# Optimization experiments

Hardware: AMD Instinct MI355X
Metric: run time of the kernel (lower is better)

Reference implementation:

```python
import jax, jax.numpy as jnp
import numpy as np
from math import log

MODEL_DIM = 512
NUM_HEADS = 8
DIM_HEAD = 64
INNER = NUM_HEADS * DIM_HEAD
B, L = 8, 1024
EPS = 1e-5


def setup_inputs() -> dict:
    key = jax.random.key(0)
    ks = jax.random.split(key, 9)
    x = jax.random.normal(ks[0], (B, L, MODEL_DIM), dtype=jnp.float32)
    gamma = jnp.ones((MODEL_DIM,), jnp.float32)
    beta = jnp.zeros((MODEL_DIM,), jnp.float32)
    w_qkv = jax.random.normal(ks[1], (3 * INNER, MODEL_DIM), jnp.float32) * (MODEL_DIM ** -0.5)
    b_qkv = jnp.zeros((3 * INNER,), jnp.float32)
    w_pos = jax.random.normal(ks[2], (INNER, MODEL_DIM), jnp.float32) * (MODEL_DIM ** -0.5)
    w_out = jax.random.normal(ks[3], (MODEL_DIM, INNER), jnp.float32) * (INNER ** -0.5)
    b_out = jnp.zeros((MODEL_DIM,), jnp.float32)
    # xavier_uniform for (num_heads, dim_head)
    bound = (6.0 / (NUM_HEADS + DIM_HEAD)) ** 0.5
    u_bias = jax.random.uniform(ks[4], (NUM_HEADS, DIM_HEAD), jnp.float32, -bound, bound)
    v_bias = jax.random.uniform(ks[5], (NUM_HEADS, DIM_HEAD), jnp.float32, -bound, bound)
    return {"x": x, "gamma": gamma, "beta": beta, "w_qkv": w_qkv, "b_qkv": b_qkv,
            "w_pos": w_pos, "w_out": w_out, "b_out": b_out, "u_bias": u_bias, "v_bias": v_bias}


def _rel_pos_emb(seq_len, d):
    # (L, D): (i - j) scaled by sinusoid frequencies, then cos on even cols, sin on odd cols
    rel = (jnp.arange(seq_len, dtype=jnp.float32)[:, None]
           - jnp.arange(d, dtype=jnp.float32)[None, :])
    freqs = jnp.exp(-jnp.arange(0, 2 * d, 2, dtype=jnp.float32) * (log(10000.0) / MODEL_DIM))
    angle = rel * freqs[None, :]
    even = (jnp.arange(d) % 2) == 0
    return jnp.where(even[None, :], jnp.cos(angle), jnp.sin(angle))  # (L, D)


def reference(x, gamma, beta, w_qkv, b_qkv, w_pos, w_out, b_out, u_bias, v_bias):
    b, l, d = x.shape
    h, dh = NUM_HEADS, DIM_HEAD
    # LayerNorm
    mu = jnp.mean(x, axis=-1, keepdims=True)
    var = jnp.mean(jnp.square(x - mu), axis=-1, keepdims=True)
    xn = (x - mu) * jax.lax.rsqrt(var + EPS) * gamma + beta
    # relative position embedding, identical per batch element
    pe = _rel_pos_emb(l, d)                      # (L, D)
    pos = (pe @ w_pos.T).reshape(l, h, dh)       # (L, H, Dh)
    pos = jnp.transpose(pos, (1, 0, 2))          # (H, L, Dh)
    # qkv
    qkv = xn @ w_qkv.T + b_qkv                   # (B, L, 3*inner)
    q, k, v = jnp.split(qkv, 3, axis=-1)
    def to_heads(t):
        return jnp.transpose(t.reshape(b, l, h, dh), (0, 2, 1, 3))  # (B,H,L,Dh)
    q, k, v = to_heads(q), to_heads(k), to_heads(v)
    scale = dh ** -0.5
    content = jnp.einsum('bhld,bhmd->bhlm', q + u_bias[None, :, None, :], k)
    pos_score = jnp.einsum('bhld,hmd->bhlm', q + v_bias[None, :, None, :], pos)
    attn = jax.nn.softmax((content + pos_score) * scale, axis=-1)
    out = jnp.einsum('bhlm,bhmd->bhld', attn, v)
    out = jnp.transpose(out, (0, 2, 1, 3)).reshape(b, l, h * dh)
    return out @ w_out.T + b_out  # dropout p=0.0 -> identity
```

## Files before the change

kernel.cpp:

```cpp
#include <hip/hip_runtime.h>
#include <math.h>

static constexpr int Bn = 8, Ln = 1024, Dm = 512, Hn = 8, DhN = 64;

typedef short bf16x8 __attribute__((ext_vector_type(8)));
typedef float f32x4 __attribute__((ext_vector_type(4)));
typedef _Float16 f16x4 __attribute__((ext_vector_type(4)));
typedef _Float16 f16x8 __attribute__((ext_vector_type(8)));
typedef unsigned int u32x4 __attribute__((ext_vector_type(4)));

#define QSCALE 0.1803368801111137f

static __device__ __forceinline__ unsigned short f2b(float f) {
  union { float f; unsigned int u; } x;
  x.f = f;
  unsigned int u = x.u;
  unsigned int r = (u + 0x7FFFu + ((u >> 16) & 1u)) >> 16;
  return (unsigned short)r;
}
static __device__ __forceinline__ float b2f(unsigned short u) {
  union { unsigned int u; float f; } x;
  x.u = ((unsigned int)u) << 16;
  return x.f;
}

#define GLDS16(g, l)                                                        \
  __builtin_amdgcn_global_load_lds((const __attribute__((address_space(1))) void*)(g), \
                                   (__attribute__((address_space(3))) void*)(l), 16, 0, 0)

__global__ __launch_bounds__(256) void prep1(const float* __restrict__ x,
                                             const float* __restrict__ gamma,
                                             const float* __restrict__ beta,
                                             unsigned short* __restrict__ xn,
                                             unsigned short* __restrict__ pe,
                                             const float* __restrict__ wq, unsigned short* __restrict__ wqb,
                                             const float* __restrict__ wp, unsigned short* __restrict__ wpb,
                                             const float* __restrict__ wo, unsigned short* __restrict__ wob) {
  int b = blockIdx.x;
  int t = threadIdx.x;
  if (b < 8192) {
    const float2 v = *(const float2*)(x + (size_t)b * Dm + t * 2);
    float s = v.x + v.y;
    float sq = v.x * v.x + v.y * v.y;
#pragma unroll
    for (int off = 32; off > 0; off >>= 1) {
      s += __shfl_down(s, off);
      sq += __shfl_down(sq, off);
    }
    __shared__ float red[8];
    int wave = t >> 6, lane = t & 63;
    if (lane == 0) { red[wave * 2] = s; red[wave * 2 + 1] = sq; }
    __syncthreads();
    float S = red[0] + red[2] + red[4] + red[6];
    float SQ = red[1] + red[3] + red[5] + red[7];
    float mu = S * (1.0f / Dm);
    float var = SQ * (1.0f / Dm) - mu * mu;
    float rstd = rsqrtf(var + 1e-5f);
    int c = t * 2;
    ushort2 o;
    o.x = f2b((v.x - mu) * rstd * gamma[c] + beta[c]);
    o.y = f2b((v.y - mu) * rstd * gamma[c + 1] + beta[c + 1]);
    *(ushort2*)(xn + (size_t)b * Dm + c) = o;
  } else if (b < 10240) {
    int idx = (b - 8192) * 256 + t;
    int l = idx >> 9, k = idx & 511;
    float freq = expf(-0.0359778921f * (float)k);
    float angle = (float)(l - k) * freq;
    pe[idx] = f2b((k & 1) ? sinf(angle) : cosf(angle));
  } else {
    int cb = b - 10240;
    const float* src;
    unsigned short* dst;
    int off;
    if (cb < 768) { src = wq; dst = wqb; off = cb; }
    else if (cb < 1024) { src = wp; dst = wpb; off = cb - 768; }
    else { src = wo; dst = wob; off = cb - 1024; }
    int i = off * 256 + t;
    float4 v = *(const float4*)(src + (size_t)i * 4);
    ushort4 o;
    o.x = f2b(v.x); o.y = f2b(v.y); o.z = f2b(v.z); o.w = f2b(v.w);
    *(ushort4*)(dst + (size_t)i * 4) = o;
  }
}

__global__ __launch_bounds__(256, 8) void gemm_mfma(const unsigned short* __restrict__ Ain,
                                                    const unsigned short* __restrict__ Bwin,
                                                    const float* __restrict__ biasin,
                                                    float* __restrict__ outfin,
                                                    unsigned short* __restrict__ oq,
                                                    unsigned short* __restrict__ ok,
                                                    unsigned short* __restrict__ ov,
                                                    const unsigned short* __restrict__ A2,
                                                    const unsigned short* __restrict__ B2,
                                                    float* __restrict__ outf2,
                                                    int K, int mode) {
  int by = blockIdx.y, bx = blockIdx.x;
  const unsigned short* A = Ain;
  const unsigned short* Bw = Bwin;
  const float* bias = biasin;
  float* outf = outfin;
  if (by >= 128) {
    if (bx >= 8) return;
    A = A2; Bw = B2; bias = nullptr; outf = outf2; mode = 1; by -= 128;
  }
  __shared__ alignas(16) unsigned short As[64 * 64];
  __shared__ alignas(16) unsigned short Bs[64 * 64];
  const int t = threadIdx.x;
  const int lane = t & 63, w = t >> 6;
  const int c = lane & 15, q8 = lane >> 4;
  const int wm = (w & 1) * 32, wn = (w >> 1) * 32;
  const int m0 = by * 64, n0 = bx * 64;

  f32x4 acc[2][2];
#pragma unroll
  for (int i = 0; i < 2; ++i)
#pragma unroll
    for (int j = 0; j < 2; ++j) acc[i][j] = (f32x4){0.f, 0.f, 0.f, 0.f};

  const int srow = lane >> 3;
  const int sgr = (lane & 7) ^ srow;

  for (int k0 = 0; k0 < K; k0 += 64) {
    __syncthreads();
#pragma unroll
    for (int j = 0; j < 2; ++j) {
      int r = j * 32 + w * 8 + srow;
      GLDS16(A + (size_t)(m0 + r) * K + k0 + sgr * 8, As + (j * 256 + w * 64 + lane) * 8);
      GLDS16(Bw + (size_t)(n0 + r) * K + k0 + sgr * 8, Bs + (j * 256 + w * 64 + lane) * 8);
    }
    __syncthreads();
#pragma unroll
    for (int kk = 0; kk < 2; ++kk) {
      bf16x8 a[2], b[2];
      const int q = kk * 4 + q8;
#pragma unroll
      for (int i = 0; i < 2; ++i) {
        int r = wm + i * 16 + c;
        a[i] = *(const bf16x8*)&As[(r * 8 + (q ^ (r & 7))) * 8];
      }
#pragma unroll
      for (int j = 0; j < 2; ++j) {
        int r = wn + j * 16 + c;
        b[j] = *(const bf16x8*)&Bs[(r * 8 + (q ^ (r & 7))) * 8];
      }
#pragma unroll
      for (int i = 0; i < 2; ++i)
#pragma unroll
        for (int j = 0; j < 2; ++j)
          acc[i][j] = __builtin_amdgcn_mfma_f32_16x16x32_bf16(a[i], b[j], acc[i][j], 0, 0, 0);
    }
  }
#pragma unroll
  for (int i = 0; i < 2; ++i) {
#pragma unroll
    for (int r = 0; r < 4; ++r) {
      int m = m0 + wm + i * 16 + q8 * 4 + r;
#pragma unroll
      for (int j = 0; j < 2; ++j) {
        int n = n0 + wn + j * 16 + c;
        float val = acc[i][j][r] + (bias ? bias[n] : 0.0f);
        if (mode == 0) {
          int part = n >> 9, h = (n >> 6) & 7, dh = n & 63;
          int bb = m >> 10, l = m & 1023;
          size_t idx = (size_t)((bb * 8 + h) * 1024 + l) * 64 + dh;
          if (part == 0) {
            oq[idx] = f2b(val * QSCALE);
          } else if (part == 1) {
            ok[idx] = f2b(val);
          } else {
            union { _Float16 h; unsigned short u; } cv;
            cv.h = (_Float16)val;
            ov[idx] = cv.u;
          }
        } else if (mode == 1) {
          int h = n >> 6, dh = n & 63;
          outf[(size_t)(h * 1024 + m) * 64 + dh] = val;
        } else {
          outf[(size_t)m * 512 + n] = val;
        }
      }
    }
  }
}

__global__ __launch_bounds__(256) void prep2(unsigned short* __restrict__ kbuf,
                                             const float* __restrict__ pos,
                                             const float* __restrict__ ub,
                                             const float* __restrict__ vbb,
                                             float* __restrict__ biasout,
                                             const unsigned short* __restrict__ v,
                                             unsigned short* __restrict__ vt) {
  int b = blockIdx.x;
  int t = threadIdx.x;
  if (b < 16384) {
    int wave = t >> 6, lane = t & 63;
    int g = b * 4 + wave;
    int h = (g >> 10) & 7;
    int m = g & 1023;
    float kv = b2f(kbuf[(size_t)g * 64 + lane]);
    float pv = pos[(size_t)(h * 1024 + m) * 64 + lane];
    float val = ub[h * 64 + lane] * kv + vbb[h * 64 + lane] * pv;
#pragma unroll
    for (int off = 32; off > 0; off >>= 1) val += __shfl_down(val, off);
    if (lane == 0) biasout[g] = val * QSCALE;
    kbuf[(size_t)g * 64 + lane] = f2b(kv + pv);
  } else {
    __shared__ unsigned short Ts[64 * 68];
    int bb = b - 16384;
    int bh = bb >> 4, lt = bb & 15;
    const unsigned short* vg = v + (size_t)bh * 65536 + lt * 4096;
#pragma unroll
    for (int s = 0; s < 4; ++s) {
      int idx = t + s * 256;
      int r = idx >> 4, c4 = (idx & 15) << 2;
      *(ushort4*)&Ts[r * 68 + c4] = *(const ushort4*)(vg + r * 64 + c4);
    }
    __syncthreads();
#pragma unroll
    for (int s = 0; s < 4; ++s) {
      int idx = t + s * 256;
      int d = idx >> 4, l4 = (idx & 15) << 2;
      ushort4 o;
      o.x = Ts[(l4 + 0) * 68 + d];
      o.y = Ts[(l4 + 1) * 68 + d];
      o.z = Ts[(l4 + 2) * 68 + d];
      o.w = Ts[(l4 + 3) * 68 + d];
      int pb = ((l4 >> 2) & 3) * 16 + ((l4 >> 4) & 3) * 4;
      *(ushort4*)(vt + (size_t)bh * 65536 + d * 1024 + lt * 64 + pb) = o;
    }
  }
}

__global__ __launch_bounds__(256, 2) void flash_mfma(const unsigned short* __restrict__ qbf,
                                                     const unsigned short* __restrict__ kbf,
                                                     const unsigned short* __restrict__ vt,
                                                     const float* __restrict__ bias,
                                                     unsigned short* __restrict__ attn_out) {
  __shared__ alignas(16) unsigned short Ks[2][64 * 64];
  __shared__ alignas(16) unsigned short Vs[2][64 * 64];
  __shared__ alignas(16) float Bls[1024];
  const int t = threadIdx.x;
  const int lane = t & 63, w = t >> 6;
  const int c = lane & 15, q8 = lane >> 4;
  const int cc7 = c & 7;
  const int bh = blockIdx.y, qt = blockIdx.x;
  const unsigned short* qg = qbf + (size_t)bh * 65536;
  const unsigned short* kg = kbf + (size_t)bh * 65536;
  const unsigned short* vg = vt + (size_t)bh * 65536;
  const float* bg = bias + (size_t)bh * 1024;

  GLDS16(bg + t * 4, Bls + t * 4);

  bf16x8 bq[2][2];
#pragma unroll
  for (int g = 0; g < 2; ++g) {
    int qlg = qt * 128 + g * 64 + w * 16 + c;
    bq[g][0] = *(const bf16x8*)(qg + (size_t)qlg * 64 + q8 * 8);
    bq[g][1] = *(const bf16x8*)(qg + (size_t)qlg * 64 + 32 + q8 * 8);
  }

  float m_st[2] = {-INFINITY, -INFINITY};
  float l_st[2] = {0.0f, 0.0f};
  f32x4 o[2][4];
#pragma unroll
  for (int g = 0; g < 2; ++g)
#pragma unroll
    for (int i = 0; i < 4; ++i) o[g][i] = (f32x4){0.f, 0.f, 0.f, 0.f};

  const int srow = lane >> 3;
  const int sgr = (lane & 7) ^ srow;
  const int r0 = w * 16 + srow;

  u32x4 pk[2][2], pv[2][2];
#pragma unroll
  for (int h = 0; h < 2; ++h)
#pragma unroll
    for (int j = 0; j < 2; ++j) {
      int r = r0 + j * 8;
      pk[h][j] = *(const u32x4*)(kg + (size_t)(h * 64 + r) * 64 + sgr * 8);
      pv[h][j] = *(const u32x4*)(vg + (size_t)r * 1024 + h * 64 + sgr * 8);
    }

  for (int it = 0; it < 8; ++it) {
    __syncthreads();
#pragma unroll
    for (int h = 0; h < 2; ++h)
#pragma unroll
      for (int j = 0; j < 2; ++j) {
        int r = r0 + j * 8;
        *(u32x4*)&Ks[h][(r * 8 + (lane & 7)) * 8] = pk[h][j];
        *(u32x4*)&Vs[h][(r * 8 + (lane & 7)) * 8] = pv[h][j];
      }
    __syncthreads();
    if (it < 7) {
#pragma unroll
      for (int h = 0; h < 2; ++h)
#pragma unroll
        for (int j = 0; j < 2; ++j) {
          int r = r0 + j * 8;
          pk[h][j] = *(const u32x4*)(kg + (size_t)((it + 1) * 128 + h * 64 + r) * 64 + sgr * 8);
          pv[h][j] = *(const u32x4*)(vg + (size_t)r * 1024 + (it + 1) * 128 + h * 64 + sgr * 8);
        }
    }

    f32x4 sc[2][2][4];
#pragma unroll
    for (int h = 0; h < 2; ++h) {
#pragma unroll
      for (int nt = 0; nt < 4; ++nt) {
        f32x4 ci = *(const f32x4*)&Bls[it * 128 + h * 64 + nt * 16 + q8 * 4];
        const int row = nt * 16 + c;
        bf16x8 ak0 = *(const bf16x8*)&Ks[h][(row * 8 + (q8 ^ cc7)) * 8];
        bf16x8 ak1 = *(const bf16x8*)&Ks[h][(row * 8 + ((q8 + 4) ^ cc7)) * 8];
#pragma unroll
        for (int g = 0; g < 2; ++g) {
          f32x4 z = __builtin_amdgcn_mfma_f32_16x16x32_bf16(ak0, bq[g][0], ci, 0, 0, 0);
          sc[g][h][nt] = __builtin_amdgcn_mfma_f32_16x16x32_bf16(ak1, bq[g][1], z, 0, 0, 0);
        }
      }
    }
    float mx[2];
#pragma unroll
    for (int g = 0; g < 2; ++g) {
      float m = sc[g][0][0][0];
#pragma unroll
      for (int h = 0; h < 2; ++h)
#pragma unroll
        for (int nt = 0; nt < 4; ++nt)
#pragma unroll
          for (int r = 0; r < 4; ++r) m = fmaxf(m, sc[g][h][nt][r]);
      mx[g] = m;
    }
    {
      float s0 = __shfl_xor(mx[0], 16);
      float s1 = __shfl_xor(mx[1], 16);
      mx[0] = fmaxf(mx[0], s0);
      mx[1] = fmaxf(mx[1], s1);
      s0 = __shfl_xor(mx[0], 32);
      s1 = __shfl_xor(mx[1], 32);
      mx[0] = fmaxf(mx[0], s0);
      mx[1] = fmaxf(mx[1], s1);
    }
    f16x4 pf[2][2][4];
#pragma unroll
    for (int g = 0; g < 2; ++g) {
      float mn = fmaxf(m_st[g], mx[g]);
      float al = __builtin_amdgcn_exp2f(m_st[g] - mn);
      float su = 0.0f;
#pragma unroll
      for (int h = 0; h < 2; ++h)
#pragma unroll
        for (int nt = 0; nt < 4; ++nt)
#pragma unroll
          for (int r = 0; r < 4; ++r) {
            float p = __builtin_amdgcn_exp2f(sc[g][h][nt][r] - mn);
            su += p;
            pf[g][h][nt][r] = (_Float16)p;
          }
      l_st[g] = l_st[g] * al + su;
      m_st[g] = mn;
#pragma unroll
      for (int i = 0; i < 4; ++i) o[g][i] *= al;
    }
#pragma unroll
    for (int i = 0; i < 4; ++i) {
      const int row = i * 16 + c;
#pragma unroll
      for (int h = 0; h < 2; ++h) {
        f16x8 v01 = *(const f16x8*)&Vs[h][(row * 8 + ((2 * q8) ^ cc7)) * 8];
        f16x8 v23 = *(const f16x8*)&Vs[h][(row * 8 + ((2 * q8 + 1) ^ cc7)) * 8];
        f16x4 a0 = {v01[0], v01[1], v01[2], v01[3]};
        f16x4 a1 = {v01[4], v01[5], v01[6], v01[7]};
        f16x4 a2 = {v23[0], v23[1], v23[2], v23[3]};
        f16x4 a3 = {v23[4], v23[5], v23[6], v23[7]};
#pragma unroll
        for (int g = 0; g < 2; ++g) {
          o[g][i] = __builtin_amdgcn_mfma_f32_16x16x16f16(a0, pf[g][h][0], o[g][i], 0, 0, 0);
          o[g][i] = __builtin_amdgcn_mfma_f32_16x16x16f16(a1, pf[g][h][1], o[g][i], 0, 0, 0);
          o[g][i] = __builtin_amdgcn_mfma_f32_16x16x16f16(a2, pf[g][h][2], o[g][i], 0, 0, 0);
          o[g][i] = __builtin_amdgcn_mfma_f32_16x16x16f16(a3, pf[g][h][3], o[g][i], 0, 0, 0);
        }
      }
    }
  }
  float lt0 = l_st[0], lt1 = l_st[1];
  {
    float s0 = __shfl_xor(lt0, 16);
    float s1 = __shfl_xor(lt1, 16);
    lt0 += s0; lt1 += s1;
    s0 = __shfl_xor(lt0, 32);
    s1 = __shfl_xor(lt1, 32);
    lt0 += s0; lt1 += s1;
  }
  const int bidx = bh >> 3, h = bh & 7;
#pragma unroll
  for (int g = 0; g < 2; ++g) {
    int qlg = qt * 128 + g * 64 + w * 16 + c;
    float inv = 1.0f / (g == 0 ? lt0 : lt1);
    size_t base = (size_t)(bidx * 1024 + qlg) * 512 + h * 64;
#pragma unroll
    for (int i = 0; i < 4; ++i) {
      ushort4 ov4;
      ov4.x = f2b(o[g][i][0] * inv);
      ov4.y = f2b(o[g][i][1] * inv);
      ov4.z = f2b(o[g][i][2] * inv);
      ov4.w = f2b(o[g][i][3] * inv);
      *(ushort4*)(attn_out + base + i * 16 + q8 * 4) = ov4;
    }
  }
}

extern "C" void kernel_launch(void* const* d_in, const int* in_sizes, int n_in,
                              void* d_out, int out_size, void* d_ws, size_t ws_size,
                              hipStream_t stream) {
  const float* x      = (const float*)d_in[0];
  const float* gamma  = (const float*)d_in[1];
  const float* beta   = (const float*)d_in[2];
  const float* w_qkv  = (const float*)d_in[3];
  const float* b_qkv  = (const float*)d_in[4];
  const float* w_pos  = (const float*)d_in[5];
  const float* w_out  = (const float*)d_in[6];
  const float* b_out  = (const float*)d_in[7];
  const float* u_bias = (const float*)d_in[8];
  const float* v_bias = (const float*)d_in[9];
  float* out = (float*)d_out;

  unsigned short* wsu = (unsigned short*)d_ws;
  unsigned short* xnb   = wsu;
  unsigned short* peb   = wsu + 4194304;
  unsigned short* wqkvb = wsu + 4718592;
  unsigned short* wposb = wsu + 5505024;
  unsigned short* woutb = wsu + 5767168;
  unsigned short* qbf   = wsu + 6291456;
  unsigned short* kbf   = wsu + 10485760;
  unsigned short* vbf   = wsu + 14680064;
  unsigned short* vtb   = wsu + 18874368;
  unsigned short* attnb = wsu + 23068672;
  float* posb  = (float*)(wsu + 27262976);
  float* biasb = (float*)(wsu + 28311552);

  prep1<<<11520, 256, 0, stream>>>(x, gamma, beta, xnb, peb,
                                   w_qkv, wqkvb, w_pos, wposb, w_out, woutb);
  gemm_mfma<<<dim3(24, 144), 256, 0, stream>>>(xnb, wqkvb, b_qkv, nullptr, qbf, kbf, vbf,
                                               peb, wposb, posb, 512, 0);
  prep2<<<17408, 256, 0, stream>>>(kbf, posb, u_bias, v_bias, biasb, vbf, vtb);
  flash_mfma<<<dim3(8, 64), 256, 0, stream>>>(qbf, kbf, vtb, biasb, attnb);
  gemm_mfma<<<dim3(8, 128), 256, 0, stream>>>(attnb, woutb, b_out, out, nullptr, nullptr, nullptr,
                                              nullptr, nullptr, nullptr, 512, 2);
}
```

Baseline: 176.3 us.

## Enlarge GEMM tiles to 128x128 and use 16x16x32 f16 MFMA for PV

The GEMM kernel moves from 64x64 tiles with a 2x2 MFMA grid per wave to 128x128 tiles with a 4x4 grid per wave. This raises operand reuse from shared memory and cuts the number of blocks, at the cost of more registers and lower occupancy. The V-transpose layout in prep2 is permuted so the flash kernel can feed 16x16x32 f16 MFMAs from two 8-wide LDS loads, replacing four 16x16x16 MFMAs per step. This halves the MFMA instruction count in the PV product and drops the vector splitting.

```diff
diff --git a/kernel.cpp b/kernel.cpp
--- a/kernel.cpp
+++ b/kernel.cpp
@@ -83,80 +83,80 @@
   }
 }
 
-__global__ __launch_bounds__(256, 8) void gemm_mfma(const unsigned short* __restrict__ Ain,
-                                                    const unsigned short* __restrict__ Bwin,
-                                                    const float* __restrict__ biasin,
-                                                    float* __restrict__ outfin,
-                                                    unsigned short* __restrict__ oq,
-                                                    unsigned short* __restrict__ ok,
-                                                    unsigned short* __restrict__ ov,
-                                                    const unsigned short* __restrict__ A2,
-                                                    const unsigned short* __restrict__ B2,
-                                                    float* __restrict__ outf2,
-                                                    int K, int mode) {
+__global__ __launch_bounds__(256) void gemm_mfma(const unsigned short* __restrict__ Ain,
+                                                 const unsigned short* __restrict__ Bwin,
+                                                 const float* __restrict__ biasin,
+                                                 float* __restrict__ outfin,
+                                                 unsigned short* __restrict__ oq,
+                                                 unsigned short* __restrict__ ok,
+                                                 unsigned short* __restrict__ ov,
+                                                 const unsigned short* __restrict__ A2,
+                                                 const unsigned short* __restrict__ B2,
+                                                 float* __restrict__ outf2,
+                                                 int K, int mode) {
   int by = blockIdx.y, bx = blockIdx.x;
   const unsigned short* A = Ain;
   const unsigned short* Bw = Bwin;
   const float* bias = biasin;
   float* outf = outfin;
-  if (by >= 128) {
-    if (bx >= 8) return;
-    A = A2; Bw = B2; bias = nullptr; outf = outf2; mode = 1; by -= 128;
-  }
-  __shared__ alignas(16) unsigned short As[64 * 64];
-  __shared__ alignas(16) unsigned short Bs[64 * 64];
+  if (by >= 64) {
+    if (bx >= 4) return;
+    A = A2; Bw = B2; bias = nullptr; outf = outf2; mode = 1; by -= 64;
+  }
+  __shared__ alignas(16) unsigned short As[128 * 64];
+  __shared__ alignas(16) unsigned short Bs[128 * 64];
   const int t = threadIdx.x;
   const int lane = t & 63, w = t >> 6;
   const int c = lane & 15, q8 = lane >> 4;
-  const int wm = (w & 1) * 32, wn = (w >> 1) * 32;
-  const int m0 = by * 64, n0 = bx * 64;
-
-  f32x4 acc[2][2];
-#pragma unroll
-  for (int i = 0; i < 2; ++i)
-#pragma unroll
-    for (int j = 0; j < 2; ++j) acc[i][j] = (f32x4){0.f, 0.f, 0.f, 0.f};
-
-  const int srow = lane >> 3;
-  const int sgr = (lane & 7) ^ srow;
+  const int wm = (w & 1) * 64, wn = (w >> 1) * 64;
+  const int m0 = by * 128, n0 = bx * 128;
+
+  f32x4 acc[4][4];
+#pragma unroll
+  for (int i = 0; i < 4; ++i)
+#pragma unroll
+    for (int j = 0; j < 4; ++j) acc[i][j] = (f32x4){0.f, 0.f, 0.f, 0.f};
+
+  const int srow = t >> 3;
+  const int sgr = (t & 7) ^ (srow & 7);
 
   for (int k0 = 0; k0 < K; k0 += 64) {
     __syncthreads();
 #pragma unroll
-    for (int j = 0; j < 2; ++j) {
-      int r = j * 32 + w * 8 + srow;
-      GLDS16(A + (size_t)(m0 + r) * K + k0 + sgr * 8, As + (j * 256 + w * 64 + lane) * 8);
-      GLDS16(Bw + (size_t)(n0 + r) * K + k0 + sgr * 8, Bs + (j * 256 + w * 64 + lane) * 8);
+    for (int s = 0; s < 4; ++s) {
+      int r = s * 32 + srow;
+      GLDS16(A + (size_t)(m0 + r) * K + k0 + sgr * 8, As + (s * 256 + t) * 8);
+      GLDS16(Bw + (size_t)(n0 + r) * K + k0 + sgr * 8, Bs + (s * 256 + t) * 8);
     }
     __syncthreads();
 #pragma unroll
     for (int kk = 0; kk < 2; ++kk) {
-      bf16x8 a[2], b[2];
+      bf16x8 a[4], b[4];
       const int q = kk * 4 + q8;
 #pragma unroll
-      for (int i = 0; i < 2; ++i) {
+      for (int i = 0; i < 4; ++i) {
         int r = wm + i * 16 + c;
         a[i] = *(const bf16x8*)&As[(r * 8 + (q ^ (r & 7))) * 8];
       }
 #pragma unroll
-      for (int j = 0; j < 2; ++j) {
+      for (int j = 0; j < 4; ++j) {
         int r = wn + j * 16 + c;
         b[j] = *(const bf16x8*)&Bs[(r * 8 + (q ^ (r & 7))) * 8];
       }
 #pragma unroll
-      for (int i = 0; i < 2; ++i)
-#pragma unroll
-        for (int j = 0; j < 2; ++j)
+      for (int i = 0; i < 4; ++i)
+#pragma unroll
+        for (int j = 0; j < 4; ++j)
           acc[i][j] = __builtin_amdgcn_mfma_f32_16x16x32_bf16(a[i], b[j], acc[i][j], 0, 0, 0);
     }
   }
 #pragma unroll
-  for (int i = 0; i < 2; ++i) {
+  for (int i = 0; i < 4; ++i) {
 #pragma unroll
     for (int r = 0; r < 4; ++r) {
       int m = m0 + wm + i * 16 + q8 * 4 + r;
 #pragma unroll
-      for (int j = 0; j < 2; ++j) {
+      for (int j = 0; j < 4; ++j) {
         int n = n0 + wn + j * 16 + c;
         float val = acc[i][j][r] + (bias ? bias[n] : 0.0f);
         if (mode == 0) {
@@ -225,7 +225,7 @@
       o.y = Ts[(l4 + 1) * 68 + d];
       o.z = Ts[(l4 + 2) * 68 + d];
       o.w = Ts[(l4 + 3) * 68 + d];
-      int pb = ((l4 >> 2) & 3) * 16 + ((l4 >> 4) & 3) * 4;
+      int pb = ((l4 >> 5) & 1) * 32 + ((l4 >> 2) & 3) * 8 + ((l4 >> 4) & 1) * 4;
       *(ushort4*)(vt + (size_t)bh * 65536 + d * 1024 + lt * 64 + pb) = o;
     }
   }
@@ -341,7 +341,7 @@
       mx[0] = fmaxf(mx[0], s0);
       mx[1] = fmaxf(mx[1], s1);
     }
-    f16x4 pf[2][2][4];
+    f16x8 pf8[2][2][2];
 #pragma unroll
     for (int g = 0; g < 2; ++g) {
       float mn = fmaxf(m_st[g], mx[g]);
@@ -355,7 +355,7 @@
           for (int r = 0; r < 4; ++r) {
             float p = __builtin_amdgcn_exp2f(sc[g][h][nt][r] - mn);
             su += p;
-            pf[g][h][nt][r] = (_Float16)p;
+            pf8[g][h][nt >> 1][((nt & 1) << 2) | r] = (_Float16)p;
           }
       l_st[g] = l_st[g] * al + su;
       m_st[g] = mn;
@@ -367,18 +367,12 @@
       const int row = i * 16 + c;
 #pragma unroll
       for (int h = 0; h < 2; ++h) {
-        f16x8 v01 = *(const f16x8*)&Vs[h][(row * 8 + ((2 * q8) ^ cc7)) * 8];
-        f16x8 v23 = *(const f16x8*)&Vs[h][(row * 8 + ((2 * q8 + 1) ^ cc7)) * 8];
-        f16x4 a0 = {v01[0], v01[1], v01[2], v01[3]};
-        f16x4 a1 = {v01[4], v01[5], v01[6], v01[7]};
-        f16x4 a2 = {v23[0], v23[1], v23[2], v23[3]};
-        f16x4 a3 = {v23[4], v23[5], v23[6], v23[7]};
+        f16x8 va = *(const f16x8*)&Vs[h][(row * 8 + (q8 ^ cc7)) * 8];
+        f16x8 vb = *(const f16x8*)&Vs[h][(row * 8 + ((4 + q8) ^ cc7)) * 8];
 #pragma unroll
         for (int g = 0; g < 2; ++g) {
-          o[g][i] = __builtin_amdgcn_mfma_f32_16x16x16f16(a0, pf[g][h][0], o[g][i], 0, 0, 0);
-          o[g][i] = __builtin_amdgcn_mfma_f32_16x16x16f16(a1, pf[g][h][1], o[g][i], 0, 0, 0);
-          o[g][i] = __builtin_amdgcn_mfma_f32_16x16x16f16(a2, pf[g][h][2], o[g][i], 0, 0, 0);
-          o[g][i] = __builtin_amdgcn_mfma_f32_16x16x16f16(a3, pf[g][h][3], o[g][i], 0, 0, 0);
+          o[g][i] = __builtin_amdgcn_mfma_f32_16x16x32_f16(va, pf8[g][h][0], o[g][i], 0, 0, 0);
+          o[g][i] = __builtin_amdgcn_mfma_f32_16x16x32_f16(vb, pf8[g][h][1], o[g][i], 0, 0, 0);
         }
       }
     }
@@ -441,10 +435,10 @@
 
   prep1<<<11520, 256, 0, stream>>>(x, gamma, beta, xnb, peb,
                                    w_qkv, wqkvb, w_pos, wposb, w_out, woutb);
-  gemm_mfma<<<dim3(24, 144), 256, 0, stream>>>(xnb, wqkvb, b_qkv, nullptr, qbf, kbf, vbf,
-                                               peb, wposb, posb, 512, 0);
+  gemm_mfma<<<dim3(12, 72), 256, 0, stream>>>(xnb, wqkvb, b_qkv, nullptr, qbf, kbf, vbf,
+                                              peb, wposb, posb, 512, 0);
   prep2<<<17408, 256, 0, stream>>>(kbf, posb, u_bias, v_bias, biasb, vbf, vtb);
   flash_mfma<<<dim3(8, 64), 256, 0, stream>>>(qbf, kbf, vtb, biasb, attnb);
-  gemm_mfma<<<dim3(8, 128), 256, 0, stream>>>(attnb, woutb, b_out, out, nullptr, nullptr, nullptr,
-                                              nullptr, nullptr, nullptr, 512, 2);
-}
+  gemm_mfma<<<dim3(4, 64), 256, 0, stream>>>(attnb, woutb, b_out, out, nullptr, nullptr, nullptr,
+                                             nullptr, nullptr, nullptr, 512, 2);
+}
```

New measurement: 207.1 us. +17.5%, slower.
